# Kernel optimization log

Hardware: AMD Instinct MI355X
Metric: run time of the kernel (lower is better)

The kernel has to match this reference:

```python
import math
import jax
import jax.numpy as jnp
import numpy as np
from jax import lax

B, L, D_MODEL, N_HEADS, C = 4, 2048, 512, 8, 1
D_HEAD = D_MODEL // N_HEADS


def setup_inputs() -> dict:
    key = jax.random.key(0)
    ks = jax.random.split(key, 7)
    s = 0.02  # stand-in for glorot init scale
    return {
        "queries": jax.random.normal(ks[0], (B, L, D_MODEL), jnp.float32),
        "keys": jax.random.normal(ks[1], (B, L, D_MODEL), jnp.float32),
        "values": jax.random.normal(ks[2], (B, L, D_MODEL), jnp.float32),
        "wq": jax.random.normal(ks[3], (D_MODEL, D_MODEL), jnp.float32) * s,
        "wk": jax.random.normal(ks[4], (D_MODEL, D_MODEL), jnp.float32) * s,
        "wv": jax.random.normal(ks[5], (D_MODEL, D_MODEL), jnp.float32) * s,
        "wo": jax.random.normal(ks[6], (D_MODEL, D_MODEL), jnp.float32) * s,
    }


def reference(queries, keys, values, wq, wk, wv, wo):
    b, len_q, _ = queries.shape
    len_k = keys.shape[1]
    # QKV projections, split into heads: [B, H, L, Dh]
    Q = (queries @ wq).reshape(b, len_q, N_HEADS, D_HEAD).transpose(0, 2, 1, 3)
    K = (keys @ wk).reshape(b, len_k, N_HEADS, D_HEAD).transpose(0, 2, 1, 3)
    V = (values @ wv).reshape(b, len_k, N_HEADS, D_HEAD).transpose(0, 2, 1, 3)
    # full O(L^2) correlation as in the original, then mean over heads & query idx
    corr = jnp.einsum("bhid,bhjd->bhij", Q, K)  # [B, H, Lq, Lk]
    mean_corr = corr.mean(axis=(1, 2))  # [B, Lk]
    # top-k delay selection (k = max(1, int(c * log(Lq))), static at trace time)
    k = max(1, int(C * math.log(max(2, len_q))))
    topk_vals, topk_idx = lax.top_k(mean_corr, k)  # [B, k]
    weights = jax.nn.softmax(topk_vals, axis=-1)  # [B, k]
    # vectorized circular roll: rolled[b,i,h,t,d] = V[b,h,(t+delay_bi) % L, d]
    idx = (jnp.arange(len_k)[None, None, :] + topk_idx[:, :, None]) % len_k  # [B,k,L]
    gathered = jnp.take_along_axis(
        V[:, None],  # [B, 1, H, L, Dh]
        idx[:, :, None, :, None],  # [B, k, 1, L, 1]
        axis=3,
    )  # [B, k, H, L, Dh]
    agg = jnp.einsum("bk,bkhld->bhld", weights.astype(V.dtype), gathered)
    out = agg.transpose(0, 2, 1, 3).reshape(b, len_q, D_MODEL) @ wo
    return out
```

## Files before the change

kernel.cpp:

```cpp
#include <hip/hip_runtime.h>
#include <hip/hip_bf16.h>

#define DMODEL 512
#define LEN 2048
#define NBATCH 4
#define TOPK 7
#define LDK 40

typedef __attribute__((ext_vector_type(8))) short short8;
typedef __attribute__((ext_vector_type(4))) float floatx4;

__device__ __forceinline__ float b2f(ushort h) {
  union { uint u; float f; } c; c.u = ((uint)h) << 16; return c.f;
}
__device__ __forceinline__ ushort f2b(float f) {
  union { float f; uint u; } c; c.f = f;
  uint u = c.u;
  uint r = (u + 0x7fffu + ((u >> 16) & 1u)) >> 16;
  return (ushort)r;
}

__device__ __forceinline__ float ld1(const void* p, size_t i, int bf) {
  return bf ? b2f(((const ushort*)p)[i]) : ((const float*)p)[i];
}
__device__ __forceinline__ void ld4v(const void* p, size_t i, int bf, float* o) {
  if (bf) {
    uint2 v = *(const uint2*)((const ushort*)p + i);
    const ushort* s = (const ushort*)&v;
#pragma unroll
    for (int j = 0; j < 4; ++j) o[j] = b2f(s[j]);
  } else {
    float4 a = *(const float4*)((const float*)p + i);
    o[0] = a.x; o[1] = a.y; o[2] = a.z; o[3] = a.w;
  }
}
__device__ __forceinline__ void ld8v(const void* p, size_t i, int bf, float* o) {
  if (bf) {
    uint4 v = *(const uint4*)((const ushort*)p + i);
    const ushort* s = (const ushort*)&v;
#pragma unroll
    for (int j = 0; j < 8; ++j) o[j] = b2f(s[j]);
  } else {
    float4 a = *(const float4*)((const float*)p + i);
    float4 b = *(const float4*)((const float*)p + i + 4);
    o[0] = a.x; o[1] = a.y; o[2] = a.z; o[3] = a.w;
    o[4] = b.x; o[5] = b.y; o[6] = b.z; o[7] = b.w;
  }
}

__device__ __forceinline__ int detect_bf16(const void* probe) {
  __shared__ int s_flag;
  int t = threadIdx.x;
  if (t < 64) {
    const uint4* p = (const uint4*)probe;
    uint4 a = p[t * 2];
    uint4 b = p[t * 2 + 1];
    uint w[8] = {a.x, a.y, a.z, a.w, b.x, b.y, b.z, b.w};
    int c = 0;
#pragma unroll
    for (int j = 0; j < 8; ++j) {
      uint e = (w[j] >> 7) & 0xFFu;
      c += (e < 90u || e > 140u) ? 1 : 0;
    }
#pragma unroll
    for (int off = 32; off > 0; off >>= 1) c += __shfl_down(c, off);
    if (t == 0) s_flag = (c < 50) ? 1 : 0;
  }
  __syncthreads();
  return s_flag;
}

__global__ __launch_bounds__(256) void prep_k(
    const void* __restrict__ queries, const void* __restrict__ values,
    const void* __restrict__ wq, const void* __restrict__ wk,
    const void* __restrict__ wv, const void* __restrict__ wo,
    float* __restrict__ P, ushort* __restrict__ VB,
    ushort* __restrict__ W2T, float* __restrict__ M) {
  __shared__ ushort As[64 * LDK];
  __shared__ ushort Bs[64 * LDK];
  __shared__ ushort Ts[64 * 72];
  int bf = detect_bf16(wq);
  int blk = blockIdx.x;
  int t = threadIdx.x;
  int w = t >> 6, lane = t & 63;
  int quad = lane >> 4, l16 = lane & 15;

  if (blk < 64) {
    int n0 = (blk & 7) * 64, m0 = (blk >> 3) * 64;
    floatx4 acc[4] = {{0,0,0,0},{0,0,0,0},{0,0,0,0},{0,0,0,0}};
    int am = t >> 2, ak = (t & 3) * 8;
    int kp = t >> 4, nb = (t & 15) * 4;
    for (int k0 = 0; k0 < DMODEL; k0 += 32) {
      float a8[8];
      ld8v(wv, (size_t)(m0 + am) * DMODEL + k0 + ak, bf, a8);
      union { ushort s[8]; uint4 v; } ap;
#pragma unroll
      for (int j = 0; j < 8; ++j) ap.s[j] = f2b(a8[j]);
      *(uint4*)(&As[am * LDK + ak]) = ap.v;
      float b0[4], b1[4];
      ld4v(wo, (size_t)(k0 + 2 * kp) * DMODEL + n0 + nb, bf, b0);
      ld4v(wo, (size_t)(k0 + 2 * kp + 1) * DMODEL + n0 + nb, bf, b1);
#pragma unroll
      for (int i = 0; i < 4; ++i) {
        ushort2 pr; pr.x = f2b(b0[i]); pr.y = f2b(b1[i]);
        *(ushort2*)(&Bs[(nb + i) * LDK + 2 * kp]) = pr;
      }
      __syncthreads();
      short8 af = *(const short8*)(&As[(w * 16 + l16) * LDK + quad * 8]);
#pragma unroll
      for (int c = 0; c < 4; ++c) {
        short8 bfr = *(const short8*)(&Bs[(c * 16 + l16) * LDK + quad * 8]);
        acc[c] = __builtin_amdgcn_mfma_f32_16x16x32_bf16(af, bfr, acc[c], 0, 0, 0);
      }
      __syncthreads();
    }
#pragma unroll
    for (int c = 0; c < 4; ++c) {
      int cl = c * 16 + l16;
#pragma unroll
      for (int r = 0; r < 4; ++r)
        Ts[cl * 72 + (w * 16 + quad * 4 + r)] = f2b(acc[c][r]);
    }
    __syncthreads();
    int nl = t >> 2, ch = t & 3;
    uint4 v0 = *(const uint4*)(&Ts[nl * 72 + ch * 16]);
    uint4 v1 = *(const uint4*)(&Ts[nl * 72 + ch * 16 + 8]);
    ushort* dst = W2T + (size_t)(n0 + nl) * DMODEL + m0 + ch * 16;
    *(uint4*)dst = v0;
    *(uint4*)(dst + 8) = v1;
  } else if (blk < 128) {
    int wb = blk - 64;
    int m0 = (wb >> 3) * 64, n0 = (wb & 7) * 64;
    floatx4 acc[4] = {{0,0,0,0},{0,0,0,0},{0,0,0,0},{0,0,0,0}};
    int am = t >> 2, ak = (t & 3) * 8;
    for (int k0 = 0; k0 < DMODEL; k0 += 32) {
      float a8[8], b8[8];
      ld8v(wk, (size_t)(m0 + am) * DMODEL + k0 + ak, bf, a8);
      ld8v(wq, (size_t)(n0 + am) * DMODEL + k0 + ak, bf, b8);
      union { ushort s[8]; uint4 v; } ap, bp;
#pragma unroll
      for (int j = 0; j < 8; ++j) { ap.s[j] = f2b(a8[j]); bp.s[j] = f2b(b8[j]); }
      *(uint4*)(&As[am * LDK + ak]) = ap.v;
      *(uint4*)(&Bs[am * LDK + ak]) = bp.v;
      __syncthreads();
      short8 af = *(const short8*)(&As[(w * 16 + l16) * LDK + quad * 8]);
#pragma unroll
      for (int c = 0; c < 4; ++c) {
        short8 bfr = *(const short8*)(&Bs[(c * 16 + l16) * LDK + quad * 8]);
        acc[c] = __builtin_amdgcn_mfma_f32_16x16x32_bf16(af, bfr, acc[c], 0, 0, 0);
      }
      __syncthreads();
    }
    int mrow = m0 + w * 16 + quad * 4;
#pragma unroll
    for (int c = 0; c < 4; ++c) {
      int col = n0 + c * 16 + l16;
#pragma unroll
      for (int r = 0; r < 4; ++r)
        M[(size_t)(mrow + r) * DMODEL + col] = acc[c][r];
    }
  } else if (blk < 384) {
    int idx = blk - 128;
    int b = idx >> 6, c = idx & 63;
    size_t base = (((size_t)b * LEN + (size_t)c * 32) << 9) + t;
    float a0 = 0.f, a1 = 0.f;
#pragma unroll 8
    for (int l = 0; l < 32; ++l) {
      a0 += ld1(queries, base + ((size_t)l << 9), bf);
      a1 += ld1(queries, base + ((size_t)l << 9) + 256, bf);
    }
    P[(size_t)idx * DMODEL + t] = a0;
    P[(size_t)idx * DMODEL + t + 256] = a1;
  } else {
    int r = (blk - 384) * 4 + w;
    float v[8];
    ld8v(values, ((size_t)r << 9) + lane * 8, bf, v);
    union { ushort o[8]; uint4 u; } pk;
#pragma unroll
    for (int j = 0; j < 8; ++j) pk.o[j] = f2b(v[j]);
    *(uint4*)(VB + ((size_t)r << 9) + lane * 8) = pk.u;
  }
}

__global__ __launch_bounds__(256) void u_all(
    const float* __restrict__ P, const float* __restrict__ M,
    float* __restrict__ U) {
  __shared__ float qs[DMODEL];
  int blk = blockIdx.x, t = threadIdx.x;
  int b = blk >> 5, g = blk & 31;
  int w = t >> 6, lane = t & 63;
  for (int d = t; d < DMODEL; d += 256) {
    float a = 0.f;
#pragma unroll
    for (int c = 0; c < 64; ++c) a += P[(size_t)(b * 64 + c) * DMODEL + d];
    qs[d] = a;
  }
  __syncthreads();
  const float* q8 = qs + lane * 8;
#pragma unroll
  for (int i = 0; i < 4; ++i) {
    int tt = g * 16 + w * 4 + i;
    const float* mr = M + (size_t)tt * DMODEL + lane * 8;
    float4 m0 = *(const float4*)mr;
    float4 m1 = *(const float4*)(mr + 4);
    float acc = m0.x * q8[0] + m0.y * q8[1] + m0.z * q8[2] + m0.w * q8[3]
              + m1.x * q8[4] + m1.y * q8[5] + m1.z * q8[6] + m1.w * q8[7];
#pragma unroll
    for (int off = 32; off > 0; off >>= 1) acc += __shfl_down(acc, off);
    if (lane == 0) U[(size_t)b * DMODEL + tt] = acc;
  }
}

__global__ __launch_bounds__(256) void mean_corr_k(
    const void* __restrict__ keys, const float* __restrict__ u,
    float* __restrict__ mc, const void* __restrict__ probe) {
  int bf = detect_bf16(probe);
  int wid = (blockIdx.x * 256 + threadIdx.x) >> 6;
  int lane = threadIdx.x & 63;
  int b = wid >> 11, j = wid & (LEN - 1);
  float kv[8];
  ld8v(keys, (((size_t)b * LEN + j) << 9) + lane * 8, bf, kv);
  const float* ub = u + (size_t)b * DMODEL + lane * 8;
  float acc = 0.f;
#pragma unroll
  for (int i = 0; i < 8; ++i) acc += kv[i] * ub[i];
#pragma unroll
  for (int off = 32; off > 0; off >>= 1) acc += __shfl_down(acc, off);
  if (lane == 0) mc[(size_t)b * LEN + j] = acc * (1.f / 16384.f);
}

__global__ __launch_bounds__(256) void mixgemm2(
    const float* __restrict__ MC, const ushort* __restrict__ VB,
    const ushort* __restrict__ W2T, void* __restrict__ out,
    const void* __restrict__ probe) {
  __shared__ __align__(16) char smem[20480];
  ushort* As = (ushort*)smem;
  ushort* Bs = (ushort*)(smem + 10240);
  int bf = detect_bf16(probe);
  int t = threadIdx.x;
  int n0 = blockIdx.x * 128, m0 = blockIdx.y * 128;
  int b = m0 >> 11;
  int w = t >> 6, lane = t & 63;
  int quad = lane >> 4, l16 = lane & 15;

  float w7[TOPK]; int dl7[TOPK];
  {
    float* vals = (float*)smem;
    float* rv  = (float*)(smem + 8192);
    int*   ri  = (int*)  (smem + 8208);
    float* bw  = (float*)(smem + 8224);
    int*   biA = (int*)  (smem + 8256);
    float* wsm = (float*)(smem + 8288);
    int*   dsm = (int*)  (smem + 8320);
    for (int i = t; i < LEN; i += 256) vals[i] = MC[(size_t)b * LEN + i];
    __syncthreads();
    for (int it = 0; it < TOPK; ++it) {
      float bv = -3.0e38f; int bi = 0;
#pragma unroll
      for (int c = 0; c < LEN / 256; ++c) {
        int i = t + c * 256;
        float v = vals[i];
        if (v > bv) { bv = v; bi = i; }
      }
#pragma unroll
      for (int off = 32; off > 0; off >>= 1) {
        float ov = __shfl_down(bv, off);
        int   oi = __shfl_down(bi, off);
        if (ov > bv || (ov == bv && oi < bi)) { bv = ov; bi = oi; }
      }
      if (lane == 0) { rv[w] = bv; ri[w] = bi; }
      __syncthreads();
      if (t == 0) {
        float fv = rv[0]; int fi = ri[0];
        for (int x = 1; x < 4; ++x)
          if (rv[x] > fv || (rv[x] == fv && ri[x] < fi)) { fv = rv[x]; fi = ri[x]; }
        bw[it] = fv; biA[it] = fi;
        vals[fi] = -3.0e38f;
      }
      __syncthreads();
    }
    if (t == 0) {
      float m = bw[0];
      float e[TOPK], s = 0.f;
#pragma unroll
      for (int i = 0; i < TOPK; ++i) { e[i] = __expf(bw[i] - m); s += e[i]; }
      float inv = 1.f / s;
#pragma unroll
      for (int i = 0; i < TOPK; ++i) { wsm[i] = e[i] * inv; dsm[i] = biA[i]; }
    }
    __syncthreads();
#pragma unroll
    for (int i = 0; i < TOPK; ++i) { w7[i] = wsm[i]; dl7[i] = dsm[i]; }
    __syncthreads();
  }

  int wr = (w & 1) * 64, wc = (w >> 1) * 64;
  floatx4 acc[4][4];
#pragma unroll
  for (int r = 0; r < 4; ++r)
#pragma unroll
    for (int c = 0; c < 4; ++c) acc[r][c] = (floatx4){0, 0, 0, 0};
  int sr = t >> 2, sc = (t & 3) * 8;
  int l_lo = (m0 & (LEN - 1)) + sr;
  const ushort* VBb = VB + ((size_t)b * LEN << 9);

  for (int k0 = 0; k0 < DMODEL; k0 += 32) {
    float a0[8] = {0,0,0,0,0,0,0,0}, a1[8] = {0,0,0,0,0,0,0,0};
#pragma unroll
    for (int i = 0; i < TOPK; ++i) {
      int s0 = (l_lo + dl7[i]) & (LEN - 1);
      int s1 = (l_lo + 64 + dl7[i]) & (LEN - 1);
      uint4 v0 = *(const uint4*)(VBb + ((size_t)s0 << 9) + k0 + sc);
      uint4 v1 = *(const uint4*)(VBb + ((size_t)s1 << 9) + k0 + sc);
      const ushort* p0 = (const ushort*)&v0;
      const ushort* p1 = (const ushort*)&v1;
      float wi = w7[i];
#pragma unroll
      for (int j = 0; j < 8; ++j) {
        a0[j] += wi * b2f(p0[j]);
        a1[j] += wi * b2f(p1[j]);
      }
    }
    union { ushort s[8]; uint4 v; } pk0, pk1;
#pragma unroll
    for (int j = 0; j < 8; ++j) { pk0.s[j] = f2b(a0[j]); pk1.s[j] = f2b(a1[j]); }
    *(uint4*)(&As[sr * LDK + sc])        = pk0.v;
    *(uint4*)(&As[(sr + 64) * LDK + sc]) = pk1.v;
    *(uint4*)(&Bs[sr * LDK + sc])        = *(const uint4*)(W2T + (size_t)(n0 + sr) * DMODEL + k0 + sc);
    *(uint4*)(&Bs[(sr + 64) * LDK + sc]) = *(const uint4*)(W2T + (size_t)(n0 + sr + 64) * DMODEL + k0 + sc);
    __syncthreads();
    short8 af[4], bfg[4];
#pragma unroll
    for (int r = 0; r < 4; ++r)
      af[r] = *(const short8*)(&As[(wr + r * 16 + l16) * LDK + quad * 8]);
#pragma unroll
    for (int c = 0; c < 4; ++c)
      bfg[c] = *(const short8*)(&Bs[(wc + c * 16 + l16) * LDK + quad * 8]);
#pragma unroll
    for (int r = 0; r < 4; ++r)
#pragma unroll
      for (int c = 0; c < 4; ++c)
        acc[r][c] = __builtin_amdgcn_mfma_f32_16x16x32_bf16(af[r], bfg[c], acc[r][c], 0, 0, 0);
    __syncthreads();
  }
#pragma unroll
  for (int r = 0; r < 4; ++r) {
    int row = m0 + wr + r * 16 + quad * 4;
#pragma unroll
    for (int c = 0; c < 4; ++c) {
      int col = n0 + wc + c * 16 + l16;
#pragma unroll
      for (int rr = 0; rr < 4; ++rr) {
        size_t oidx = (size_t)(row + rr) * DMODEL + col;
        float v = acc[r][c][rr];
        if (bf) ((ushort*)out)[oidx] = f2b(v);
        else    ((float*)out)[oidx] = v;
      }
    }
  }
}

extern "C" void kernel_launch(void* const* d_in, const int* in_sizes, int n_in,
                              void* d_out, int out_size, void* d_ws, size_t ws_size,
                              hipStream_t stream) {
  const void* queries = d_in[0];
  const void* keys    = d_in[1];
  const void* values  = d_in[2];
  const void* wq      = d_in[3];
  const void* wk      = d_in[4];
  const void* wv      = d_in[5];
  const void* wo      = d_in[6];

  char* ws = (char*)d_ws;
  float*  P    = (float*)(ws + 0);
  ushort* W2T  = (ushort*)(ws + 524288);
  float*  M    = (float*)(ws + 1048576);
  float*  U    = (float*)(ws + 2097152);
  float*  MC   = (float*)(ws + 2105344);
  ushort* VB   = (ushort*)(ws + 4194304);

  prep_k<<<2432, 256, 0, stream>>>(queries, values, wq, wk, wv, wo, P, VB, W2T, M);
  u_all<<<128, 256, 0, stream>>>(P, M, U);
  mean_corr_k<<<NBATCH * LEN / 4, 256, 0, stream>>>(keys, U, MC, wq);
  mixgemm2<<<dim3(4, 64), 256, 0, stream>>>(MC, VB, W2T, d_out, wq);
}
```

Before: 162.8 us.

## Double mixgemm2 block to 512 threads and batch the top-k gather loads

Runs the fused top-k/mix/GEMM kernel with 512 threads per block. Each thread now stages one A row and one B row instead of two, and the waves are split into 4x2 tiles of 32x64. The seven delayed-row pointers are precomputed once, and all seven gather loads are issued together before the weighted sum, to expose memory-level parallelism. This trades more waves per block and a little extra shared memory for fewer accumulators per wave and shorter serial gather chains.

Result: no change. 163.0 us (+0.1%).

```diff
diff --git a/kernel.cpp b/kernel.cpp
--- a/kernel.cpp
+++ b/kernel.cpp
@@ -229,11 +229,11 @@
   if (lane == 0) mc[(size_t)b * LEN + j] = acc * (1.f / 16384.f);
 }
 
-__global__ __launch_bounds__(256) void mixgemm2(
+__global__ __launch_bounds__(512) void mixgemm2(
     const float* __restrict__ MC, const ushort* __restrict__ VB,
     const ushort* __restrict__ W2T, void* __restrict__ out,
     const void* __restrict__ probe) {
-  __shared__ __align__(16) char smem[20480];
+  __shared__ __align__(16) char smem[20992];
   ushort* As = (ushort*)smem;
   ushort* Bs = (ushort*)(smem + 10240);
   int bf = detect_bf16(probe);
@@ -247,18 +247,18 @@
   {
     float* vals = (float*)smem;
     float* rv  = (float*)(smem + 8192);
-    int*   ri  = (int*)  (smem + 8208);
-    float* bw  = (float*)(smem + 8224);
-    int*   biA = (int*)  (smem + 8256);
-    float* wsm = (float*)(smem + 8288);
-    int*   dsm = (int*)  (smem + 8320);
-    for (int i = t; i < LEN; i += 256) vals[i] = MC[(size_t)b * LEN + i];
+    int*   ri  = (int*)  (smem + 8224);
+    float* bw  = (float*)(smem + 8256);
+    int*   biA = (int*)  (smem + 8288);
+    float* wsm = (float*)(smem + 8320);
+    int*   dsm = (int*)  (smem + 8352);
+    for (int i = t; i < LEN; i += 512) vals[i] = MC[(size_t)b * LEN + i];
     __syncthreads();
     for (int it = 0; it < TOPK; ++it) {
       float bv = -3.0e38f; int bi = 0;
 #pragma unroll
-      for (int c = 0; c < LEN / 256; ++c) {
-        int i = t + c * 256;
+      for (int c = 0; c < LEN / 512; ++c) {
+        int i = t + c * 512;
         float v = vals[i];
         if (v > bv) { bv = v; bi = i; }
       }
@@ -272,7 +272,7 @@
       __syncthreads();
       if (t == 0) {
         float fv = rv[0]; int fi = ri[0];
-        for (int x = 1; x < 4; ++x)
+        for (int x = 1; x < 8; ++x)
           if (rv[x] > fv || (rv[x] == fv && ri[x] < fi)) { fv = rv[x]; fi = ri[x]; }
         bw[it] = fv; biA[it] = fi;
         vals[fi] = -3.0e38f;
@@ -294,57 +294,54 @@
     __syncthreads();
   }
 
-  int wr = (w & 1) * 64, wc = (w >> 1) * 64;
-  floatx4 acc[4][4];
-#pragma unroll
-  for (int r = 0; r < 4; ++r)
+  int wr = (w & 3) * 32, wc = (w >> 2) * 64;
+  floatx4 acc[2][4];
+#pragma unroll
+  for (int r = 0; r < 2; ++r)
 #pragma unroll
     for (int c = 0; c < 4; ++c) acc[r][c] = (floatx4){0, 0, 0, 0};
   int sr = t >> 2, sc = (t & 3) * 8;
-  int l_lo = (m0 & (LEN - 1)) + sr;
+  int l_me = (m0 & (LEN - 1)) + sr;
   const ushort* VBb = VB + ((size_t)b * LEN << 9);
+  const ushort* srcp[TOPK];
+#pragma unroll
+  for (int i = 0; i < TOPK; ++i)
+    srcp[i] = VBb + ((size_t)((l_me + dl7[i]) & (LEN - 1)) << 9) + sc;
 
   for (int k0 = 0; k0 < DMODEL; k0 += 32) {
-    float a0[8] = {0,0,0,0,0,0,0,0}, a1[8] = {0,0,0,0,0,0,0,0};
+    uint4 g[TOPK];
+#pragma unroll
+    for (int i = 0; i < TOPK; ++i) g[i] = *(const uint4*)(srcp[i] + k0);
+    float a8[8] = {0,0,0,0,0,0,0,0};
 #pragma unroll
     for (int i = 0; i < TOPK; ++i) {
-      int s0 = (l_lo + dl7[i]) & (LEN - 1);
-      int s1 = (l_lo + 64 + dl7[i]) & (LEN - 1);
-      uint4 v0 = *(const uint4*)(VBb + ((size_t)s0 << 9) + k0 + sc);
-      uint4 v1 = *(const uint4*)(VBb + ((size_t)s1 << 9) + k0 + sc);
-      const ushort* p0 = (const ushort*)&v0;
-      const ushort* p1 = (const ushort*)&v1;
+      const ushort* p = (const ushort*)&g[i];
       float wi = w7[i];
 #pragma unroll
-      for (int j = 0; j < 8; ++j) {
-        a0[j] += wi * b2f(p0[j]);
-        a1[j] += wi * b2f(p1[j]);
-      }
-    }
-    union { ushort s[8]; uint4 v; } pk0, pk1;
-#pragma unroll
-    for (int j = 0; j < 8; ++j) { pk0.s[j] = f2b(a0[j]); pk1.s[j] = f2b(a1[j]); }
-    *(uint4*)(&As[sr * LDK + sc])        = pk0.v;
-    *(uint4*)(&As[(sr + 64) * LDK + sc]) = pk1.v;
-    *(uint4*)(&Bs[sr * LDK + sc])        = *(const uint4*)(W2T + (size_t)(n0 + sr) * DMODEL + k0 + sc);
-    *(uint4*)(&Bs[(sr + 64) * LDK + sc]) = *(const uint4*)(W2T + (size_t)(n0 + sr + 64) * DMODEL + k0 + sc);
-    __syncthreads();
-    short8 af[4], bfg[4];
-#pragma unroll
-    for (int r = 0; r < 4; ++r)
+      for (int j = 0; j < 8; ++j) a8[j] += wi * b2f(p[j]);
+    }
+    union { ushort s[8]; uint4 v; } pk;
+#pragma unroll
+    for (int j = 0; j < 8; ++j) pk.s[j] = f2b(a8[j]);
+    *(uint4*)(&As[sr * LDK + sc]) = pk.v;
+    *(uint4*)(&Bs[sr * LDK + sc]) = *(const uint4*)(W2T + (size_t)(n0 + sr) * DMODEL + k0 + sc);
+    __syncthreads();
+    short8 af[2], bfg[4];
+#pragma unroll
+    for (int r = 0; r < 2; ++r)
       af[r] = *(const short8*)(&As[(wr + r * 16 + l16) * LDK + quad * 8]);
 #pragma unroll
     for (int c = 0; c < 4; ++c)
       bfg[c] = *(const short8*)(&Bs[(wc + c * 16 + l16) * LDK + quad * 8]);
 #pragma unroll
-    for (int r = 0; r < 4; ++r)
+    for (int r = 0; r < 2; ++r)
 #pragma unroll
       for (int c = 0; c < 4; ++c)
         acc[r][c] = __builtin_amdgcn_mfma_f32_16x16x32_bf16(af[r], bfg[c], acc[r][c], 0, 0, 0);
     __syncthreads();
   }
 #pragma unroll
-  for (int r = 0; r < 4; ++r) {
+  for (int r = 0; r < 2; ++r) {
     int row = m0 + wr + r * 16 + quad * 4;
 #pragma unroll
     for (int c = 0; c < 4; ++c) {
@@ -382,5 +379,5 @@
   prep_k<<<2432, 256, 0, stream>>>(queries, values, wq, wk, wv, wo, P, VB, W2T, M);
   u_all<<<128, 256, 0, stream>>>(P, M, U);
   mean_corr_k<<<NBATCH * LEN / 4, 256, 0, stream>>>(keys, U, MC, wq);
-  mixgemm2<<<dim3(4, 64), 256, 0, stream>>>(MC, VB, W2T, d_out, wq);
-}
+  mixgemm2<<<dim3(4, 64), 512, 0, stream>>>(MC, VB, W2T, d_out, wq);
+}
```
